# Optimization experiments

Measured on AMD Instinct MI355X. Metric: run time of the kernel, lower is better.

The kernel has to match this reference:

```python
import jax, jax.numpy as jnp
import numpy as np

NUM_CLASSES = 33  # labels 0..32; class 0 = background, 32 instances
EPS = 1e-06


def _lovasz_hinge_flat(logits, labels):
    # logits, labels: flat 1-D float arrays (labels in {0,1})
    signs = 2.0 * labels - 1.0
    errors = 1.0 - logits * signs
    order = jnp.argsort(-errors)            # descending sort
    errors_sorted = errors[order]
    gt_sorted = labels[order]
    gts = jnp.sum(gt_sorted)
    intersection = gts - jnp.cumsum(gt_sorted)
    union = gts + jnp.cumsum(1.0 - gt_sorted)
    jaccard = 1.0 - intersection / union
    grad = jnp.concatenate([jaccard[:1], jaccard[1:] - jaccard[:-1]])
    return jnp.dot(jax.nn.relu(errors_sorted), grad)


def _per_sample_loss(y_emb, y_sig, gt_patch):
    # y_emb: [2,H,W] float, y_sig: [1,H,W] float, gt_patch: [1,H,W] int
    # to_onehot(gt)[0, 1:] -> [N,H,W], N = NUM_CLASSES-1 instance channels
    gt_one_hot = jax.nn.one_hot(gt_patch[0], NUM_CLASSES, axis=0, dtype=y_emb.dtype)[1:]
    counts = jnp.sum(gt_one_hot, axis=(1, 2), keepdims=True)          # [N,1,1]
    # per-instance embedding centers: [2,N,1,1]
    centers = jnp.sum(gt_one_hot[None] * y_emb[:, None], axis=(2, 3), keepdims=True) / counts
    instance_sigmas = gt_one_hot[None] * y_sig[:, None]               # [1,N,H,W]
    sigmas = jnp.sum(instance_sigmas, axis=(2, 3), keepdims=True) / counts  # [1,N,1,1]
    var_sigmas = jnp.sum(((instance_sigmas - jax.lax.stop_gradient(sigmas)) * gt_one_hot) ** 2) / counts  # [N,1,1]
    center_dist = jnp.linalg.norm(centers - y_emb[:, None], axis=0)   # [N,H,W]
    probs = jnp.exp(-0.5 * (center_dist / sigmas) ** 2)               # [1,N,H,W]
    logits = (probs * 2.0 - 1.0).reshape(-1)
    labels = jnp.broadcast_to(gt_one_hot[None], probs.shape).reshape(-1)
    return _lovasz_hinge_flat(logits, labels) + jnp.mean(var_sigmas)


def setup_inputs() -> dict:
    key = jax.random.key(0)
    k1, k2, k3 = jax.random.split(key, 3)
    B, H, W = 4, 512, 512
    y_embeddings = jax.random.normal(k1, (B, 2, H, W), dtype=jnp.float32)
    y_sigma = jax.random.uniform(k2, (B, 1, H, W), dtype=jnp.float32)
    y_true = jax.random.randint(k3, (B, 1, H, W), 0, NUM_CLASSES, dtype=jnp.int64)
    return {"y_embeddings": y_embeddings, "y_sigma": y_sigma, "y_true": y_true}


def reference(y_embeddings, y_sigma, y_true):
    # Assumes every sample contains foreground (random labels over 512x512
    # guarantee this w.h.p.), so the torch `if torch.any(gt>0)` branch is taken
    # for all samples and the final loss is the mean over the batch.
    losses = jax.vmap(_per_sample_loss)(y_embeddings, y_sigma, y_true)
    return jnp.mean(losses)
```

## Files before the change

### kernel.cpp

```cpp
#include <hip/hip_runtime.h>

#define HW    262144
#define BNUM  4
#define NC    33
#define NI    32

#define NB     2048
#define BSCALE 128.0f
#define EG     8192
#define ESCALE 4096.0f

typedef unsigned long long ull;

#define W_TH   0
#define W_E0   4096
#define W_E1   (W_E0 + NC)
#define W_SS   (W_E1 + NC)
#define W_SS2  (W_SS + NC)
#define W_CNT  (W_SS2 + NC)
#define W_STRIDE 4262
#define W_FIN  (BNUM * W_STRIDE)
#define WS_ZERO_BYTES ((W_FIN + 8) * 4)

__global__ void __launch_bounds__(256) stats_kernel(
    const float* __restrict__ emb, const float* __restrict__ sig,
    const int* __restrict__ gt, float* __restrict__ ws) {
  int s = blockIdx.y;
  float* wsS = ws + (size_t)s * W_STRIDE;
  __shared__ float a0[4][NC], a1[4][NC], as_[4][NC], as2[4][NC];
  __shared__ unsigned ac[4][NC];
  int t = threadIdx.x;
  int w = t >> 6;
  for (int k = t; k < 4 * NC; k += 256) {
    ((float*)a0)[k] = 0.f; ((float*)a1)[k] = 0.f;
    ((float*)as_)[k] = 0.f; ((float*)as2)[k] = 0.f;
    ((unsigned*)ac)[k] = 0u;
  }
  __syncthreads();
  const float* e0p = emb + (size_t)s * 2 * HW;
  const float* e1p = e0p + HW;
  const float* sp  = sig + (size_t)s * HW;
  const int*   gp  = gt  + (size_t)s * HW;
  int idx = blockIdx.x * 1024 + t * 4;
  int4   lb = *(const int4*)(gp + idx);
  float4 x  = *(const float4*)(e0p + idx);
  float4 y  = *(const float4*)(e1p + idx);
  float4 sg = *(const float4*)(sp + idx);
#define ACC(L, X, Y, SG)                                              \
  if (L > 0) {                                                        \
    atomicAdd(&a0[w][L], X); atomicAdd(&a1[w][L], Y);                 \
    atomicAdd(&as_[w][L], SG); atomicAdd(&as2[w][L], (SG) * (SG));    \
    atomicAdd(&ac[w][L], 1u);                                         \
  }
  ACC(lb.x, x.x, y.x, sg.x)
  ACC(lb.y, x.y, y.y, sg.y)
  ACC(lb.z, x.z, y.z, sg.z)
  ACC(lb.w, x.w, y.w, sg.w)
#undef ACC
  __syncthreads();
  if (t >= 1 && t < NC) {
    float s0 = a0[0][t] + a0[1][t] + a0[2][t] + a0[3][t];
    float s1 = a1[0][t] + a1[1][t] + a1[2][t] + a1[3][t];
    float ss = as_[0][t] + as_[1][t] + as_[2][t] + as_[3][t];
    float s2 = as2[0][t] + as2[1][t] + as2[2][t] + as2[3][t];
    unsigned c = ac[0][t] + ac[1][t] + ac[2][t] + ac[3][t];
    if (c) {
      atomicAdd(&wsS[W_E0 + t], s0);
      atomicAdd(&wsS[W_E1 + t], s1);
      atomicAdd(&wsS[W_SS + t], ss);
      atomicAdd(&wsS[W_SS2 + t], s2);
      atomicAdd((unsigned*)wsS + (W_CNT + t), c);
    }
  }
}

__global__ void __launch_bounds__(512) hist_kernel(
    const float* __restrict__ emb, const int* __restrict__ gt,
    float* __restrict__ ws) {
  int s = blockIdx.y;
  float* wsS = ws + (size_t)s * W_STRIDE;
  __shared__ unsigned hist[NB * 4];
  __shared__ float4 cons[NC];
  int t = threadIdx.x;
  int r = t & 3;
  for (int k = t; k < NB * 4; k += 512) hist[k] = 0u;
  if (t >= 1 && t < NC) {
    float inv = 1.0f / (float)((const unsigned*)wsS)[W_CNT + t];
    float c0 = wsS[W_E0 + t] * inv;
    float c1 = wsS[W_E1 + t] * inv;
    float sgm = wsS[W_SS + t] * inv;
    float Q = 0.5f / (sgm * sgm) * BSCALE;
    float4 c;
    c.x = Q;
    c.y = -2.0f * Q * c0;
    c.z = -2.0f * Q * c1;
    c.w = Q * (c0 * c0 + c1 * c1);
    cons[t] = c;
  }
  __syncthreads();
  const float* e0p = emb + (size_t)s * 2 * HW;
  const float* e1p = e0p + HW;
  const int*   gp  = gt  + (size_t)s * HW;
  int idx = blockIdx.x * 2048 + t * 4;
  int4   lb = *(const int4*)(gp + idx);
  float4 px = *(const float4*)(e0p + idx);
  float4 py = *(const float4*)(e1p + idx);
  float4 ss;
  ss.x = fmaf(px.x, px.x, py.x * py.x);
  ss.y = fmaf(px.y, px.y, py.y * py.y);
  ss.z = fmaf(px.z, px.z, py.z * py.z);
  ss.w = fmaf(px.w, px.w, py.w * py.w);
  unsigned* hr = hist + r;
  #pragma unroll 4
  for (int n = 1; n <= NI; ++n) {
    float4 C = cons[n];
#define ITEM(P0, P1, SV, L)                                            \
    {                                                                  \
      float bf = fmaf(C.x, SV, fmaf(C.y, P0, fmaf(C.z, P1, C.w)));     \
      int ib = (int)bf;                                                \
      bool pos = (L == n);                                             \
      if (pos) ib = min(ib, NB - 1);                                   \
      if (ib < NB) atomicAdd(&hr[ib << 2], pos ? 0x10000u : 1u);       \
    }
    ITEM(px.x, py.x, ss.x, lb.x)
    ITEM(px.y, py.y, ss.y, lb.y)
    ITEM(px.z, py.z, ss.z, lb.z)
    ITEM(px.w, py.w, ss.w, lb.w)
#undef ITEM
  }
  __syncthreads();
  ull* th = (ull*)wsS;
  for (int k = t; k < NB; k += 512) {
    unsigned v = hist[k * 4] + hist[k * 4 + 1] + hist[k * 4 + 2] + hist[k * 4 + 3];
    if (v) {
      ull add = ((ull)(v >> 16) << 32) | (v & 0xFFFFu);
      atomicAdd(&th[k], add);
    }
  }
}

__global__ void __launch_bounds__(512) scan_kernel(
    float* __restrict__ ws, float* __restrict__ out) {
  int s = blockIdx.x;
  float* wsS = ws + (size_t)s * W_STRIDE;
  const ull* th = (const ull*)wsS;
  const unsigned* wsu = (const unsigned*)wsS;
  __shared__ unsigned ep[EG], en[EG];
  __shared__ ull wsum[8];
  __shared__ float red[8];
  __shared__ float vart_s;
  int t = threadIdx.x;
  int lane = t & 63, wid = t >> 6;
  for (int k = t; k < EG; k += 512) { ep[k] = 0u; en[k] = 0u; }
  if (wid == 0) {
    float S = 0.f, rc = 0.f;
    if (lane >= 1 && lane < NC) {
      float c = (float)wsu[W_CNT + lane];
      float sg = wsS[W_SS + lane] / c;
      S = wsS[W_SS2 + lane] - c * sg * sg;
      rc = 1.0f / c;
    }
    for (int o = 32; o; o >>= 1) {
      S  += __shfl_down(S, o);
      rc += __shfl_down(rc, o);
    }
    if (lane == 0) vart_s = S * rc / (float)NI;
  }
  __syncthreads();
  for (int b = t; b < NB; b += 512) {
    ull v = th[b];
    unsigned pos = (unsigned)(v >> 32), neg = (unsigned)(v & 0xFFFFFFFFu);
    if (pos | neg) {
      float tc = ((float)b + 0.5f) * (1.0f / BSCALE);
      float ex = __expf(-tc);
      if (pos) {
        float e = 2.0f - 2.0f * ex;
        int k = (int)(e * ESCALE); if (k > EG - 1) k = EG - 1;
        atomicAdd(&ep[k], pos);
      }
      if (neg) {
        float e = 2.0f * ex;
        int k = (int)(e * ESCALE); if (k > EG - 1) k = EG - 1;
        atomicAdd(&en[k], neg);
      }
    }
  }
  __syncthreads();
  const int CH = EG / 512;
  int j0 = t * CH;
  unsigned np = 0, nn = 0;
  for (int k = 0; k < CH; ++k) {
    int b = EG - 1 - (j0 + k);
    np += ep[b]; nn += en[b];
  }
  ull v = ((ull)np << 32) | (ull)nn;
  ull inc = v;
  for (int o = 1; o < 64; o <<= 1) {
    ull u = __shfl_up(inc, o);
    if (lane >= o) inc += u;
  }
  if (lane == 63) wsum[wid] = inc;
  __syncthreads();
  ull offset = 0, total = 0;
  for (int i = 0; i < 8; ++i) {
    ull x = wsum[i];
    if (i < wid) offset += x;
    total += x;
  }
  ull excl = offset + inc - v;
  float P = (float)(unsigned)(total >> 32);
  unsigned p = (unsigned)(excl >> 32), f = (unsigned)(excl & 0xFFFFFFFFu);
  float jprev = 1.0f - (P - (float)p) / (P + (float)f);
  float contrib = 0.f;
  for (int k = 0; k < CH; ++k) {
    int b = EG - 1 - (j0 + k);
    unsigned ap_ = ep[b], an_ = en[b];
    if (ap_ | an_) {
      p += ap_; f += an_;
      float j = 1.0f - (P - (float)p) / (P + (float)f);
      float e = ((float)b + 0.5f) * (2.0f / EG);
      contrib += e * (j - jprev);
      jprev = j;
    }
  }
  for (int o = 32; o; o >>= 1) contrib += __shfl_down(contrib, o);
  if (lane == 0) red[wid] = contrib;
  __syncthreads();
  if (t == 0) {
    float tot = 0.f;
    for (int i = 0; i < 8; ++i) tot += red[i];
    float loss = tot + vart_s;
    float* fin = ws + W_FIN;
    unsigned* cnt = (unsigned*)(fin + 4);
    atomicExch(&fin[s], loss);
    unsigned old = atomicAdd(cnt, 1u);
    if (old == BNUM - 1) {
      float a = 0.f;
      for (int i = 0; i < BNUM; ++i) a += atomicAdd(&fin[i], 0.0f);
      out[0] = a * (1.0f / BNUM);
    }
  }
}

extern "C" void kernel_launch(void* const* d_in, const int* in_sizes, int n_in,
                              void* d_out, int out_size, void* d_ws, size_t ws_size,
                              hipStream_t stream) {
  const float* emb = (const float*)d_in[0];
  const float* sig = (const float*)d_in[1];
  const int*   gt  = (const int*)d_in[2];
  float* out = (float*)d_out;
  float* ws  = (float*)d_ws;

  hipMemsetAsync(d_ws, 0, WS_ZERO_BYTES, stream);

  dim3 gA(256, BNUM);
  stats_kernel<<<gA, 256, 0, stream>>>(emb, sig, gt, ws);
  dim3 gB(128, BNUM);
  hist_kernel<<<gB, 512, 0, stream>>>(emb, gt, ws);
  scan_kernel<<<BNUM, 512, 0, stream>>>(ws, out);
}
```

Baseline: 126.0 us.

## Fuse memset, stats, histogram and scan into one cooperative grid-synced kernel

Replaces the memset and three separate kernel launches with a single cooperative kernel of 512 blocks that zeroes the workspace, accumulates per-instance stats, builds the distance histogram, and runs the Lovasz scan, separated by grid.sync barriers. Embedding and label tiles are loaded once and kept in registers for both the stats and histogram phases, and shared memory is reused through a union. The error-grid resolution is halved, which shrinks the scan work. This targets launch overhead and the repeated global reads, at the cost of cooperative-launch constraints, three grid-wide barriers, and a coarser loss approximation.

```diff
diff --git a/kernel.cpp b/kernel.cpp
--- a/kernel.cpp
+++ b/kernel.cpp
@@ -1,4 +1,6 @@
 #include <hip/hip_runtime.h>
+#include <hip/hip_cooperative_groups.h>
+namespace cg = cooperative_groups;
 
 #define HW    262144
 #define BNUM  4
@@ -7,8 +9,8 @@
 
 #define NB     2048
 #define BSCALE 128.0f
-#define EG     8192
-#define ESCALE 4096.0f
+#define EG     4096
+#define ESCALE 2048.0f
 
 typedef unsigned long long ull;
 
@@ -20,70 +22,74 @@
 #define W_CNT  (W_SS2 + NC)
 #define W_STRIDE 4262
 #define W_FIN  (BNUM * W_STRIDE)
-#define WS_ZERO_BYTES ((W_FIN + 8) * 4)
-
-__global__ void __launch_bounds__(256) stats_kernel(
+#define NWORDS (W_FIN + 8)
+
+union SMem {
+  struct { float a0[8][NC], a1[8][NC], as1[8][NC], as2[8][NC]; unsigned ac[8][NC]; } a;
+  struct { unsigned hist[NB * 4]; float4 cons[NC]; } b;
+  struct { unsigned ep[EG], en[EG]; ull wsum[8]; float red[8]; float vart; } c;
+};
+
+__global__ void __launch_bounds__(512, 4) fused_kernel(
     const float* __restrict__ emb, const float* __restrict__ sig,
-    const int* __restrict__ gt, float* __restrict__ ws) {
-  int s = blockIdx.y;
+    const int* __restrict__ gt, float* __restrict__ ws,
+    float* __restrict__ out) {
+  cg::grid_group grid = cg::this_grid();
+  __shared__ SMem sm;
+  int t = threadIdx.x;
+  int bid = blockIdx.x;
+  int s = bid >> 7;
+  int lb = bid & 127;
   float* wsS = ws + (size_t)s * W_STRIDE;
-  __shared__ float a0[4][NC], a1[4][NC], as_[4][NC], as2[4][NC];
-  __shared__ unsigned ac[4][NC];
-  int t = threadIdx.x;
-  int w = t >> 6;
-  for (int k = t; k < 4 * NC; k += 256) {
-    ((float*)a0)[k] = 0.f; ((float*)a1)[k] = 0.f;
-    ((float*)as_)[k] = 0.f; ((float*)as2)[k] = 0.f;
-    ((unsigned*)ac)[k] = 0u;
-  }
-  __syncthreads();
+
+  int gid = bid * 512 + t;
+  if (gid < NWORDS) ((unsigned*)ws)[gid] = 0u;
+  for (int k = t; k < 8 * NC * 5; k += 512) ((float*)&sm.a)[k] = 0.f;
+  __syncthreads();
+
   const float* e0p = emb + (size_t)s * 2 * HW;
   const float* e1p = e0p + HW;
   const float* sp  = sig + (size_t)s * HW;
   const int*   gp  = gt  + (size_t)s * HW;
-  int idx = blockIdx.x * 1024 + t * 4;
-  int4   lb = *(const int4*)(gp + idx);
-  float4 x  = *(const float4*)(e0p + idx);
-  float4 y  = *(const float4*)(e1p + idx);
-  float4 sg = *(const float4*)(sp + idx);
-#define ACC(L, X, Y, SG)                                              \
-  if (L > 0) {                                                        \
-    atomicAdd(&a0[w][L], X); atomicAdd(&a1[w][L], Y);                 \
-    atomicAdd(&as_[w][L], SG); atomicAdd(&as2[w][L], (SG) * (SG));    \
-    atomicAdd(&ac[w][L], 1u);                                         \
-  }
-  ACC(lb.x, x.x, y.x, sg.x)
-  ACC(lb.y, x.y, y.y, sg.y)
-  ACC(lb.z, x.z, y.z, sg.z)
-  ACC(lb.w, x.w, y.w, sg.w)
+  int w = t >> 6;
+  int idx = lb * 2048 + t * 4;
+  int4   lbl = *(const int4*)(gp + idx);
+  float4 x   = *(const float4*)(e0p + idx);
+  float4 y   = *(const float4*)(e1p + idx);
+  float4 sg4 = *(const float4*)(sp + idx);
+#define ACC(L, X, Y, SG)                                                  \
+  if (L > 0) {                                                            \
+    atomicAdd(&sm.a.a0[w][L], X);  atomicAdd(&sm.a.a1[w][L], Y);          \
+    atomicAdd(&sm.a.as1[w][L], SG); atomicAdd(&sm.a.as2[w][L], (SG)*(SG));\
+    atomicAdd(&sm.a.ac[w][L], 1u);                                        \
+  }
+  ACC(lbl.x, x.x, y.x, sg4.x)
+  ACC(lbl.y, x.y, y.y, sg4.y)
+  ACC(lbl.z, x.z, y.z, sg4.z)
+  ACC(lbl.w, x.w, y.w, sg4.w)
 #undef ACC
   __syncthreads();
+  float r0 = 0.f, r1 = 0.f, r2 = 0.f, r3 = 0.f;
+  unsigned rc = 0u;
   if (t >= 1 && t < NC) {
-    float s0 = a0[0][t] + a0[1][t] + a0[2][t] + a0[3][t];
-    float s1 = a1[0][t] + a1[1][t] + a1[2][t] + a1[3][t];
-    float ss = as_[0][t] + as_[1][t] + as_[2][t] + as_[3][t];
-    float s2 = as2[0][t] + as2[1][t] + as2[2][t] + as2[3][t];
-    unsigned c = ac[0][t] + ac[1][t] + ac[2][t] + ac[3][t];
-    if (c) {
-      atomicAdd(&wsS[W_E0 + t], s0);
-      atomicAdd(&wsS[W_E1 + t], s1);
-      atomicAdd(&wsS[W_SS + t], ss);
-      atomicAdd(&wsS[W_SS2 + t], s2);
-      atomicAdd((unsigned*)wsS + (W_CNT + t), c);
-    }
-  }
-}
-
-__global__ void __launch_bounds__(512) hist_kernel(
-    const float* __restrict__ emb, const int* __restrict__ gt,
-    float* __restrict__ ws) {
-  int s = blockIdx.y;
-  float* wsS = ws + (size_t)s * W_STRIDE;
-  __shared__ unsigned hist[NB * 4];
-  __shared__ float4 cons[NC];
-  int t = threadIdx.x;
-  int r = t & 3;
-  for (int k = t; k < NB * 4; k += 512) hist[k] = 0u;
+    #pragma unroll
+    for (int i = 0; i < 8; ++i) {
+      r0 += sm.a.a0[i][t]; r1 += sm.a.a1[i][t];
+      r2 += sm.a.as1[i][t]; r3 += sm.a.as2[i][t];
+      rc += sm.a.ac[i][t];
+    }
+  }
+  grid.sync();
+  if (rc) {
+    atomicAdd(&wsS[W_E0 + t], r0);
+    atomicAdd(&wsS[W_E1 + t], r1);
+    atomicAdd(&wsS[W_SS + t], r2);
+    atomicAdd(&wsS[W_SS2 + t], r3);
+    atomicAdd((unsigned*)wsS + (W_CNT + t), rc);
+  }
+  grid.sync();
+
+  for (int k = t; k < NB * 4; k += 512) sm.b.hist[k] = 0u;
   if (t >= 1 && t < NC) {
     float inv = 1.0f / (float)((const unsigned*)wsS)[W_CNT + t];
     float c0 = wsS[W_E0 + t] * inv;
@@ -95,25 +101,18 @@
     c.y = -2.0f * Q * c0;
     c.z = -2.0f * Q * c1;
     c.w = Q * (c0 * c0 + c1 * c1);
-    cons[t] = c;
-  }
-  __syncthreads();
-  const float* e0p = emb + (size_t)s * 2 * HW;
-  const float* e1p = e0p + HW;
-  const int*   gp  = gt  + (size_t)s * HW;
-  int idx = blockIdx.x * 2048 + t * 4;
-  int4   lb = *(const int4*)(gp + idx);
-  float4 px = *(const float4*)(e0p + idx);
-  float4 py = *(const float4*)(e1p + idx);
+    sm.b.cons[t] = c;
+  }
+  __syncthreads();
   float4 ss;
-  ss.x = fmaf(px.x, px.x, py.x * py.x);
-  ss.y = fmaf(px.y, px.y, py.y * py.y);
-  ss.z = fmaf(px.z, px.z, py.z * py.z);
-  ss.w = fmaf(px.w, px.w, py.w * py.w);
-  unsigned* hr = hist + r;
+  ss.x = fmaf(x.x, x.x, y.x * y.x);
+  ss.y = fmaf(x.y, x.y, y.y * y.y);
+  ss.z = fmaf(x.z, x.z, y.z * y.z);
+  ss.w = fmaf(x.w, x.w, y.w * y.w);
+  unsigned* hr = sm.b.hist + (t & 3);
   #pragma unroll 4
   for (int n = 1; n <= NI; ++n) {
-    float4 C = cons[n];
+    float4 C = sm.b.cons[n];
 #define ITEM(P0, P1, SV, L)                                            \
     {                                                                  \
       float bf = fmaf(C.x, SV, fmaf(C.y, P0, fmaf(C.z, P1, C.w)));     \
@@ -122,49 +121,45 @@
       if (pos) ib = min(ib, NB - 1);                                   \
       if (ib < NB) atomicAdd(&hr[ib << 2], pos ? 0x10000u : 1u);       \
     }
-    ITEM(px.x, py.x, ss.x, lb.x)
-    ITEM(px.y, py.y, ss.y, lb.y)
-    ITEM(px.z, py.z, ss.z, lb.z)
-    ITEM(px.w, py.w, ss.w, lb.w)
+    ITEM(x.x, y.x, ss.x, lbl.x)
+    ITEM(x.y, y.y, ss.y, lbl.y)
+    ITEM(x.z, y.z, ss.z, lbl.z)
+    ITEM(x.w, y.w, ss.w, lbl.w)
 #undef ITEM
   }
   __syncthreads();
-  ull* th = (ull*)wsS;
-  for (int k = t; k < NB; k += 512) {
-    unsigned v = hist[k * 4] + hist[k * 4 + 1] + hist[k * 4 + 2] + hist[k * 4 + 3];
-    if (v) {
-      ull add = ((ull)(v >> 16) << 32) | (v & 0xFFFFu);
-      atomicAdd(&th[k], add);
-    }
-  }
-}
-
-__global__ void __launch_bounds__(512) scan_kernel(
-    float* __restrict__ ws, float* __restrict__ out) {
-  int s = blockIdx.x;
-  float* wsS = ws + (size_t)s * W_STRIDE;
-  const ull* th = (const ull*)wsS;
-  const unsigned* wsu = (const unsigned*)wsS;
-  __shared__ unsigned ep[EG], en[EG];
-  __shared__ ull wsum[8];
-  __shared__ float red[8];
-  __shared__ float vart_s;
-  int t = threadIdx.x;
+  {
+    ull* th = (ull*)wsS;
+    for (int k = t; k < NB; k += 512) {
+      unsigned v = sm.b.hist[k*4] + sm.b.hist[k*4+1] + sm.b.hist[k*4+2] + sm.b.hist[k*4+3];
+      if (v) {
+        ull add = ((ull)(v >> 16) << 32) | (v & 0xFFFFu);
+        atomicAdd(&th[k], add);
+      }
+    }
+  }
+  grid.sync();
+
+  if (bid >= BNUM) return;
+  int sc = bid;
+  float* wsC = ws + (size_t)sc * W_STRIDE;
+  const ull* th = (const ull*)wsC;
+  const unsigned* wsu = (const unsigned*)wsC;
   int lane = t & 63, wid = t >> 6;
-  for (int k = t; k < EG; k += 512) { ep[k] = 0u; en[k] = 0u; }
+  for (int k = t; k < EG; k += 512) { sm.c.ep[k] = 0u; sm.c.en[k] = 0u; }
   if (wid == 0) {
-    float S = 0.f, rc = 0.f;
+    float S = 0.f, rcp = 0.f;
     if (lane >= 1 && lane < NC) {
       float c = (float)wsu[W_CNT + lane];
-      float sg = wsS[W_SS + lane] / c;
-      S = wsS[W_SS2 + lane] - c * sg * sg;
-      rc = 1.0f / c;
+      float sg = wsC[W_SS + lane] / c;
+      S = wsC[W_SS2 + lane] - c * sg * sg;
+      rcp = 1.0f / c;
     }
     for (int o = 32; o; o >>= 1) {
-      S  += __shfl_down(S, o);
-      rc += __shfl_down(rc, o);
-    }
-    if (lane == 0) vart_s = S * rc / (float)NI;
+      S   += __shfl_down(S, o);
+      rcp += __shfl_down(rcp, o);
+    }
+    if (lane == 0) sm.c.vart = S * rcp / (float)NI;
   }
   __syncthreads();
   for (int b = t; b < NB; b += 512) {
@@ -176,12 +171,12 @@
       if (pos) {
         float e = 2.0f - 2.0f * ex;
         int k = (int)(e * ESCALE); if (k > EG - 1) k = EG - 1;
-        atomicAdd(&ep[k], pos);
+        atomicAdd(&sm.c.ep[k], pos);
       }
       if (neg) {
         float e = 2.0f * ex;
         int k = (int)(e * ESCALE); if (k > EG - 1) k = EG - 1;
-        atomicAdd(&en[k], neg);
+        atomicAdd(&sm.c.en[k], neg);
       }
     }
   }
@@ -191,7 +186,7 @@
   unsigned np = 0, nn = 0;
   for (int k = 0; k < CH; ++k) {
     int b = EG - 1 - (j0 + k);
-    np += ep[b]; nn += en[b];
+    np += sm.c.ep[b]; nn += sm.c.en[b];
   }
   ull v = ((ull)np << 32) | (ull)nn;
   ull inc = v;
@@ -199,13 +194,13 @@
     ull u = __shfl_up(inc, o);
     if (lane >= o) inc += u;
   }
-  if (lane == 63) wsum[wid] = inc;
+  if (lane == 63) sm.c.wsum[wid] = inc;
   __syncthreads();
   ull offset = 0, total = 0;
   for (int i = 0; i < 8; ++i) {
-    ull x = wsum[i];
-    if (i < wid) offset += x;
-    total += x;
+    ull xr = sm.c.wsum[i];
+    if (i < wid) offset += xr;
+    total += xr;
   }
   ull excl = offset + inc - v;
   float P = (float)(unsigned)(total >> 32);
@@ -214,7 +209,7 @@
   float contrib = 0.f;
   for (int k = 0; k < CH; ++k) {
     int b = EG - 1 - (j0 + k);
-    unsigned ap_ = ep[b], an_ = en[b];
+    unsigned ap_ = sm.c.ep[b], an_ = sm.c.en[b];
     if (ap_ | an_) {
       p += ap_; f += an_;
       float j = 1.0f - (P - (float)p) / (P + (float)f);
@@ -224,15 +219,15 @@
     }
   }
   for (int o = 32; o; o >>= 1) contrib += __shfl_down(contrib, o);
-  if (lane == 0) red[wid] = contrib;
+  if (lane == 0) sm.c.red[wid] = contrib;
   __syncthreads();
   if (t == 0) {
     float tot = 0.f;
-    for (int i = 0; i < 8; ++i) tot += red[i];
-    float loss = tot + vart_s;
+    for (int i = 0; i < 8; ++i) tot += sm.c.red[i];
+    float loss = tot + sm.c.vart;
     float* fin = ws + W_FIN;
     unsigned* cnt = (unsigned*)(fin + 4);
-    atomicExch(&fin[s], loss);
+    atomicExch(&fin[sc], loss);
     unsigned old = atomicAdd(cnt, 1u);
     if (old == BNUM - 1) {
       float a = 0.f;
@@ -251,11 +246,7 @@
   float* out = (float*)d_out;
   float* ws  = (float*)d_ws;
 
-  hipMemsetAsync(d_ws, 0, WS_ZERO_BYTES, stream);
-
-  dim3 gA(256, BNUM);
-  stats_kernel<<<gA, 256, 0, stream>>>(emb, sig, gt, ws);
-  dim3 gB(128, BNUM);
-  hist_kernel<<<gB, 512, 0, stream>>>(emb, gt, ws);
-  scan_kernel<<<BNUM, 512, 0, stream>>>(ws, out);
+  void* args[] = {(void*)&emb, (void*)&sig, (void*)&gt, (void*)&ws, (void*)&out};
+  hipLaunchCooperativeKernel((const void*)fused_kernel, dim3(512), dim3(512),
+                             args, 0, stream);
 }
```

Result: slower. 250.7 us (+98.9%).

## Fuse histogram and scan kernels, drop memset, use per-block partials

Applied to the files above, without the earlier changes.

Removes the memset by having stats blocks zero the workspace themselves. Stats blocks now write non-atomic per-block partial sums, which the histogram blocks reduce on load. The scan is folded into the histogram kernel: the last-arriving block per sample, detected with an atomic counter, does the scan. The error grid is halved to fit in the reused shared histogram, which coarsens the Lovasz error quantisation slightly.

```diff
diff --git a/kernel.cpp b/kernel.cpp
--- a/kernel.cpp
+++ b/kernel.cpp
@@ -7,110 +7,109 @@
 
 #define NB     2048
 #define BSCALE 128.0f
-#define EG     8192
-#define ESCALE 4096.0f
+#define EG     4096
+#define ESCALE 2048.0f
 
 typedef unsigned long long ull;
 
-#define W_TH   0
-#define W_E0   4096
-#define W_E1   (W_E0 + NC)
-#define W_SS   (W_E1 + NC)
-#define W_SS2  (W_SS + NC)
-#define W_CNT  (W_SS2 + NC)
-#define W_STRIDE 4262
-#define W_FIN  (BNUM * W_STRIDE)
-#define WS_ZERO_BYTES ((W_FIN + 8) * 4)
+#define W_PART 16384
+#define W_FIN  (W_PART + 5 * 33 * 256)
 
 __global__ void __launch_bounds__(256) stats_kernel(
     const float* __restrict__ emb, const float* __restrict__ sig,
     const int* __restrict__ gt, float* __restrict__ ws) {
   int s = blockIdx.y;
-  float* wsS = ws + (size_t)s * W_STRIDE;
-  __shared__ float a0[4][NC], a1[4][NC], as_[4][NC], as2[4][NC];
-  __shared__ unsigned ac[4][NC];
+  int j = blockIdx.x;
   int t = threadIdx.x;
   int w = t >> 6;
-  for (int k = t; k < 4 * NC; k += 256) {
-    ((float*)a0)[k] = 0.f; ((float*)a1)[k] = 0.f;
-    ((float*)as_)[k] = 0.f; ((float*)as2)[k] = 0.f;
-    ((unsigned*)ac)[k] = 0u;
-  }
+  __shared__ float acc[4][165];
+  int bid = s * 64 + j;
+  unsigned* wsu = (unsigned*)ws;
+  if (t < 64) wsu[bid * 64 + t] = 0u;
+  if (bid == 0 && t < 16) wsu[W_FIN + t] = 0u;
+  for (int k = t; k < 4 * 165; k += 256) ((float*)acc)[k] = 0.f;
   __syncthreads();
   const float* e0p = emb + (size_t)s * 2 * HW;
   const float* e1p = e0p + HW;
   const float* sp  = sig + (size_t)s * HW;
   const int*   gp  = gt  + (size_t)s * HW;
-  int idx = blockIdx.x * 1024 + t * 4;
-  int4   lb = *(const int4*)(gp + idx);
-  float4 x  = *(const float4*)(e0p + idx);
-  float4 y  = *(const float4*)(e1p + idx);
-  float4 sg = *(const float4*)(sp + idx);
-#define ACC(L, X, Y, SG)                                              \
-  if (L > 0) {                                                        \
-    atomicAdd(&a0[w][L], X); atomicAdd(&a1[w][L], Y);                 \
-    atomicAdd(&as_[w][L], SG); atomicAdd(&as2[w][L], (SG) * (SG));    \
-    atomicAdd(&ac[w][L], 1u);                                         \
-  }
-  ACC(lb.x, x.x, y.x, sg.x)
-  ACC(lb.y, x.y, y.y, sg.y)
-  ACC(lb.z, x.z, y.z, sg.z)
-  ACC(lb.w, x.w, y.w, sg.w)
+  #pragma unroll
+  for (int i = 0; i < 4; ++i) {
+    int idx = j * 4096 + i * 1024 + t * 4;
+    int4   lb = *(const int4*)(gp + idx);
+    float4 x  = *(const float4*)(e0p + idx);
+    float4 y  = *(const float4*)(e1p + idx);
+    float4 sg = *(const float4*)(sp + idx);
+#define ACC(L, X, Y, SG)                                                   \
+    if (L > 0) {                                                           \
+      atomicAdd(&acc[w][L], X);        atomicAdd(&acc[w][33 + L], Y);      \
+      atomicAdd(&acc[w][66 + L], SG);  atomicAdd(&acc[w][99 + L], (SG)*(SG)); \
+      atomicAdd(&acc[w][132 + L], 1.0f);                                   \
+    }
+    ACC(lb.x, x.x, y.x, sg.x)
+    ACC(lb.y, x.y, y.y, sg.y)
+    ACC(lb.z, x.z, y.z, sg.z)
+    ACC(lb.w, x.w, y.w, sg.w)
 #undef ACC
+  }
+  __syncthreads();
+  if (t < 165) {
+    float v = acc[0][t] + acc[1][t] + acc[2][t] + acc[3][t];
+    ws[W_PART + t * 256 + s * 64 + j] = v;
+  }
+}
+
+__global__ void __launch_bounds__(512) hist_scan_kernel(
+    const float* __restrict__ emb, const int* __restrict__ gt,
+    float* __restrict__ ws, float* __restrict__ out) {
+  int s  = blockIdx.y;
+  int lb = blockIdx.x;
+  __shared__ unsigned hist[NB * 4];
+  __shared__ float sums[165];
+  __shared__ float4 cons[NC];
+  __shared__ ull wsum[8];
+  __shared__ float red[8];
+  __shared__ float vart_s;
+  __shared__ int flag;
+  int t = threadIdx.x;
+  int lane = t & 63, wid = t >> 6;
+  for (int k = t; k < NB * 4; k += 512) hist[k] = 0u;
+  if (t < 165) {
+    const float4* pp = (const float4*)(ws + W_PART + t * 256 + s * 64);
+    float sum = 0.f;
+    #pragma unroll
+    for (int i = 0; i < 16; ++i) { float4 v = pp[i]; sum += v.x + v.y + v.z + v.w; }
+    sums[t] = sum;
+  }
   __syncthreads();
   if (t >= 1 && t < NC) {
-    float s0 = a0[0][t] + a0[1][t] + a0[2][t] + a0[3][t];
-    float s1 = a1[0][t] + a1[1][t] + a1[2][t] + a1[3][t];
-    float ss = as_[0][t] + as_[1][t] + as_[2][t] + as_[3][t];
-    float s2 = as2[0][t] + as2[1][t] + as2[2][t] + as2[3][t];
-    unsigned c = ac[0][t] + ac[1][t] + ac[2][t] + ac[3][t];
-    if (c) {
-      atomicAdd(&wsS[W_E0 + t], s0);
-      atomicAdd(&wsS[W_E1 + t], s1);
-      atomicAdd(&wsS[W_SS + t], ss);
-      atomicAdd(&wsS[W_SS2 + t], s2);
-      atomicAdd((unsigned*)wsS + (W_CNT + t), c);
-    }
-  }
-}
-
-__global__ void __launch_bounds__(512) hist_kernel(
-    const float* __restrict__ emb, const int* __restrict__ gt,
-    float* __restrict__ ws) {
-  int s = blockIdx.y;
-  float* wsS = ws + (size_t)s * W_STRIDE;
-  __shared__ unsigned hist[NB * 4];
-  __shared__ float4 cons[NC];
-  int t = threadIdx.x;
-  int r = t & 3;
-  for (int k = t; k < NB * 4; k += 512) hist[k] = 0u;
-  if (t >= 1 && t < NC) {
-    float inv = 1.0f / (float)((const unsigned*)wsS)[W_CNT + t];
-    float c0 = wsS[W_E0 + t] * inv;
-    float c1 = wsS[W_E1 + t] * inv;
-    float sgm = wsS[W_SS + t] * inv;
-    float Q = 0.5f / (sgm * sgm) * BSCALE;
-    float4 c;
-    c.x = Q;
-    c.y = -2.0f * Q * c0;
-    c.z = -2.0f * Q * c1;
-    c.w = Q * (c0 * c0 + c1 * c1);
-    cons[t] = c;
+    float c = sums[132 + t];
+    float4 C;
+    if (c > 0.f) {
+      float inv = 1.0f / c;
+      float c0 = sums[t] * inv, c1 = sums[33 + t] * inv, sgm = sums[66 + t] * inv;
+      float Q = 0.5f / (sgm * sgm) * BSCALE;
+      C.x = Q; C.y = -2.0f * Q * c0; C.z = -2.0f * Q * c1;
+      C.w = Q * (c0 * c0 + c1 * c1);
+    } else {
+      C.x = 0.f; C.y = 0.f; C.z = 0.f; C.w = (float)NB;
+    }
+    cons[t] = C;
   }
   __syncthreads();
   const float* e0p = emb + (size_t)s * 2 * HW;
   const float* e1p = e0p + HW;
   const int*   gp  = gt  + (size_t)s * HW;
-  int idx = blockIdx.x * 2048 + t * 4;
-  int4   lb = *(const int4*)(gp + idx);
-  float4 px = *(const float4*)(e0p + idx);
-  float4 py = *(const float4*)(e1p + idx);
+  int idx = lb * 2048 + t * 4;
+  int4   lbl = *(const int4*)(gp + idx);
+  float4 px  = *(const float4*)(e0p + idx);
+  float4 py  = *(const float4*)(e1p + idx);
   float4 ss;
   ss.x = fmaf(px.x, px.x, py.x * py.x);
   ss.y = fmaf(px.y, px.y, py.y * py.y);
   ss.z = fmaf(px.z, px.z, py.z * py.z);
   ss.w = fmaf(px.w, px.w, py.w * py.w);
-  unsigned* hr = hist + r;
+  unsigned* hr = hist + (t & 3);
   #pragma unroll 4
   for (int n = 1; n <= NI; ++n) {
     float4 C = cons[n];
@@ -122,53 +121,52 @@
       if (pos) ib = min(ib, NB - 1);                                   \
       if (ib < NB) atomicAdd(&hr[ib << 2], pos ? 0x10000u : 1u);       \
     }
-    ITEM(px.x, py.x, ss.x, lb.x)
-    ITEM(px.y, py.y, ss.y, lb.y)
-    ITEM(px.z, py.z, ss.z, lb.z)
-    ITEM(px.w, py.w, ss.w, lb.w)
+    ITEM(px.x, py.x, ss.x, lbl.x)
+    ITEM(px.y, py.y, ss.y, lbl.y)
+    ITEM(px.z, py.z, ss.z, lbl.z)
+    ITEM(px.w, py.w, ss.w, lbl.w)
 #undef ITEM
   }
   __syncthreads();
-  ull* th = (ull*)wsS;
+  ull* th = ((ull*)ws) + (size_t)s * NB;
   for (int k = t; k < NB; k += 512) {
-    unsigned v = hist[k * 4] + hist[k * 4 + 1] + hist[k * 4 + 2] + hist[k * 4 + 3];
+    unsigned v = hist[k*4] + hist[k*4+1] + hist[k*4+2] + hist[k*4+3];
     if (v) {
       ull add = ((ull)(v >> 16) << 32) | (v & 0xFFFFu);
       atomicAdd(&th[k], add);
     }
   }
-}
-
-__global__ void __launch_bounds__(512) scan_kernel(
-    float* __restrict__ ws, float* __restrict__ out) {
-  int s = blockIdx.x;
-  float* wsS = ws + (size_t)s * W_STRIDE;
-  const ull* th = (const ull*)wsS;
-  const unsigned* wsu = (const unsigned*)wsS;
-  __shared__ unsigned ep[EG], en[EG];
-  __shared__ ull wsum[8];
-  __shared__ float red[8];
-  __shared__ float vart_s;
-  int t = threadIdx.x;
-  int lane = t & 63, wid = t >> 6;
-  for (int k = t; k < EG; k += 512) { ep[k] = 0u; en[k] = 0u; }
+  __syncthreads();
+  if (t == 0) {
+    __threadfence();
+    unsigned* cnt = (unsigned*)(ws + W_FIN);
+    flag = (atomicAdd(&cnt[8 + s], 1u) == 127u);
+  }
+  __syncthreads();
+  if (!flag) return;
+
+  unsigned* ep = hist;
+  unsigned* en = hist + EG;
+  for (int k = t; k < 2 * EG; k += 512) hist[k] = 0u;
   if (wid == 0) {
-    float S = 0.f, rc = 0.f;
+    float S = 0.f, rcp = 0.f;
     if (lane >= 1 && lane < NC) {
-      float c = (float)wsu[W_CNT + lane];
-      float sg = wsS[W_SS + lane] / c;
-      S = wsS[W_SS2 + lane] - c * sg * sg;
-      rc = 1.0f / c;
+      float c = sums[132 + lane];
+      if (c > 0.f) {
+        float sg = sums[66 + lane] / c;
+        S = sums[99 + lane] - c * sg * sg;
+        rcp = 1.0f / c;
+      }
     }
     for (int o = 32; o; o >>= 1) {
-      S  += __shfl_down(S, o);
-      rc += __shfl_down(rc, o);
-    }
-    if (lane == 0) vart_s = S * rc / (float)NI;
+      S   += __shfl_down(S, o);
+      rcp += __shfl_down(rcp, o);
+    }
+    if (lane == 0) vart_s = S * rcp / (float)NI;
   }
   __syncthreads();
   for (int b = t; b < NB; b += 512) {
-    ull v = th[b];
+    ull v = atomicAdd(&th[b], 0ull);
     unsigned pos = (unsigned)(v >> 32), neg = (unsigned)(v & 0xFFFFFFFFu);
     if (pos | neg) {
       float tc = ((float)b + 0.5f) * (1.0f / BSCALE);
@@ -203,9 +201,9 @@
   __syncthreads();
   ull offset = 0, total = 0;
   for (int i = 0; i < 8; ++i) {
-    ull x = wsum[i];
-    if (i < wid) offset += x;
-    total += x;
+    ull xr = wsum[i];
+    if (i < wid) offset += xr;
+    total += xr;
   }
   ull excl = offset + inc - v;
   float P = (float)(unsigned)(total >> 32);
@@ -233,7 +231,7 @@
     float* fin = ws + W_FIN;
     unsigned* cnt = (unsigned*)(fin + 4);
     atomicExch(&fin[s], loss);
-    unsigned old = atomicAdd(cnt, 1u);
+    unsigned old = atomicAdd(&cnt[0], 1u);
     if (old == BNUM - 1) {
       float a = 0.f;
       for (int i = 0; i < BNUM; ++i) a += atomicAdd(&fin[i], 0.0f);
@@ -251,11 +249,8 @@
   float* out = (float*)d_out;
   float* ws  = (float*)d_ws;
 
-  hipMemsetAsync(d_ws, 0, WS_ZERO_BYTES, stream);
-
-  dim3 gA(256, BNUM);
+  dim3 gA(64, BNUM);
   stats_kernel<<<gA, 256, 0, stream>>>(emb, sig, gt, ws);
   dim3 gB(128, BNUM);
-  hist_kernel<<<gB, 512, 0, stream>>>(emb, gt, ws);
-  scan_kernel<<<BNUM, 512, 0, stream>>>(ws, out);
+  hist_scan_kernel<<<gB, 512, 0, stream>>>(emb, gt, ws, out);
 }
```

Result: faster. 120.6 us (-4.3%).
